# Kernel tuning notes

Measured on AMD Instinct MI355X. Metric: run time of the kernel, lower is better.

The kernel has to match this reference:

```python
import jax, jax.numpy as jnp
import numpy as np

A = 1.0
B = 0.001


def setup_inputs() -> dict:
    key = jax.random.key(0)
    k1, k2 = jax.random.split(key)
    N, C = 4096, 50257
    pred = jax.random.normal(k1, (N, C), dtype=jnp.float32)
    labels = jax.random.randint(k2, (N,), 0, C, dtype=jnp.int64)
    return {"pred": pred, "labels": labels}


def reference(pred, labels):
    N, C = pred.shape
    rows = jnp.arange(N)
    label_logit = pred[rows, labels]  # [N]

    # Cross-entropy (mean reduction, matching nn.CrossEntropyLoss)
    logZ = jax.nn.logsumexp(pred, axis=1)  # [N]
    ce = jnp.mean(logZ - label_logit)

    # Per-row variance-sum over all non-label classes, without building
    # the [N, C] mask / [N, C-1] gather: use sum / sum-of-squares identities.
    # sum_{j != y} (x_j - mu)^2 = sumsq_neg - (C-1) * mu^2
    row_sum = jnp.sum(pred, axis=1) - label_logit            # [N]
    row_sumsq = jnp.sum(pred * pred, axis=1) - label_logit ** 2  # [N]
    m = C - 1
    mu = row_sum / m
    neg_var_sum = jnp.sum(row_sumsq - m * mu * mu)

    return A * ce + B * neg_var_sum
```

## Files before the change

### kernel.cpp

```cpp
#include <hip/hip_runtime.h>
#include <hip/hip_bf16.h>
#include <stdint.h>

#define A_COEF 1.0f
#define B_COEF 0.001f

__device__ __forceinline__ void wave_reduce3(float& a, float& b, float& c) {
    for (int off = 32; off > 0; off >>= 1) {
        a += __shfl_down(a, off);
        b += __shfl_down(b, off);
        c += __shfl_down(c, off);
    }
}

__global__ __launch_bounds__(256) void row_pass_kernel(
    const float* __restrict__ pred, const int* __restrict__ labels,
    float* __restrict__ row_out, int C, float invN) {
    const int row = blockIdx.x;
    const float* __restrict__ p = pred + (size_t)row * (size_t)C;

    const uintptr_t addr = (uintptr_t)p;
    const int head = (int)(((16u - (unsigned)(addr & 15u)) & 15u) >> 2);
    const int nvec = (C - head) >> 2;
    const int tail_start = head + (nvec << 2);

    float sum = 0.0f, ssq = 0.0f, sexp = 0.0f;
    const int t = threadIdx.x;

    for (int i = t; i < head; i += 256) {
        float x = p[i];
        sum += x; ssq = fmaf(x, x, ssq); sexp += __expf(x);
    }
    for (int i = tail_start + t; i < C; i += 256) {
        float x = p[i];
        sum += x; ssq = fmaf(x, x, ssq); sexp += __expf(x);
    }

    const float4* __restrict__ pv = (const float4*)(p + head);
    for (int k = t; k < nvec; k += 256) {
        float4 v = pv[k];
        sum += (v.x + v.y) + (v.z + v.w);
        ssq = fmaf(v.x, v.x, ssq);
        ssq = fmaf(v.y, v.y, ssq);
        ssq = fmaf(v.z, v.z, ssq);
        ssq = fmaf(v.w, v.w, ssq);
        sexp += (__expf(v.x) + __expf(v.y)) + (__expf(v.z) + __expf(v.w));
    }

    __shared__ float s_sum[4], s_ssq[4], s_sexp[4];
    wave_reduce3(sum, ssq, sexp);
    const int wave = t >> 6, lane = t & 63;
    if (lane == 0) { s_sum[wave] = sum; s_ssq[wave] = ssq; s_sexp[wave] = sexp; }
    __syncthreads();

    if (t == 0) {
        float S = 0.0f, Q = 0.0f, E = 0.0f;
        #pragma unroll
        for (int w = 0; w < 4; ++w) { S += s_sum[w]; Q += s_ssq[w]; E += s_sexp[w]; }

        const int label = labels[row];
        const float ll = p[label];

        const float logZ = logf(E);
        const float ce_i = logZ - ll;

        const float m = (float)(C - 1);
        const float rsum = S - ll;
        const float rssq = Q - ll * ll;
        const float mu = rsum / m;
        const float nv = rssq - m * mu * mu;

        row_out[row] = A_COEF * invN * ce_i + B_COEF * nv;
    }
}

__global__ __launch_bounds__(256) void final_reduce_kernel(
    const float* __restrict__ row_out, float* __restrict__ out, int n) {
    double acc = 0.0;
    for (int i = threadIdx.x; i < n; i += 256) acc += (double)row_out[i];
    for (int off = 32; off > 0; off >>= 1) acc += __shfl_down(acc, off);
    __shared__ double sd[4];
    const int wave = threadIdx.x >> 6, lane = threadIdx.x & 63;
    if (lane == 0) sd[wave] = acc;
    __syncthreads();
    if (threadIdx.x == 0) {
        double tot = 0.0;
        #pragma unroll
        for (int w = 0; w < 4; ++w) tot += sd[w];
        out[0] = (float)tot;
    }
}

extern "C" void kernel_launch(void* const* d_in, const int* in_sizes, int n_in,
                              void* d_out, int out_size, void* d_ws, size_t ws_size,
                              hipStream_t stream) {
    const float* pred = (const float*)d_in[0];
    const int* labels = (const int*)d_in[1];
    float* out = (float*)d_out;

    const int N = in_sizes[1];
    const int C = (int)((long long)in_sizes[0] / (long long)N);

    float* row_out = (float*)d_ws;

    row_pass_kernel<<<N, 256, 0, stream>>>(pred, labels, row_out, C, 1.0f / (float)N);
    final_reduce_kernel<<<1, 256, 0, stream>>>(row_out, out, N);
}
```

Before: 150.1 us.

## Fuse final reduction via fixed-point atomics and unroll nontemporal row loads

Removes the second reduction kernel. Each block now adds its row contribution to a 64-bit fixed-point accumulator with an atomic and bumps a counter, and the last block to finish writes the result. The main loop is unrolled by two with separate accumulators and uses nontemporal vector loads, to expose more memory-level parallelism and avoid cache pollution. This adds a memset launch and atomics, and the fixed-point scale limits the precision of each contribution.

```diff
diff --git a/kernel.cpp b/kernel.cpp
--- a/kernel.cpp
+++ b/kernel.cpp
@@ -4,6 +4,9 @@
 
 #define A_COEF 1.0f
 #define B_COEF 0.001f
+#define FIXED_SCALE 16777216.0
+
+typedef __attribute__((ext_vector_type(4))) float f32x4;
 
 __device__ __forceinline__ void wave_reduce3(float& a, float& b, float& c) {
     for (int off = 32; off > 0; off >>= 1) {
@@ -15,7 +18,8 @@
 
 __global__ __launch_bounds__(256) void row_pass_kernel(
     const float* __restrict__ pred, const int* __restrict__ labels,
-    float* __restrict__ row_out, int C, float invN) {
+    unsigned long long* __restrict__ ws, float* __restrict__ out,
+    int C, float invN) {
     const int row = blockIdx.x;
     const float* __restrict__ p = pred + (size_t)row * (size_t)C;
 
@@ -24,28 +28,42 @@
     const int nvec = (C - head) >> 2;
     const int tail_start = head + (nvec << 2);
 
-    float sum = 0.0f, ssq = 0.0f, sexp = 0.0f;
     const int t = threadIdx.x;
+    float sum0 = 0.0f, ssq0 = 0.0f, sexp0 = 0.0f;
+    float sum1 = 0.0f, ssq1 = 0.0f, sexp1 = 0.0f;
 
     for (int i = t; i < head; i += 256) {
         float x = p[i];
-        sum += x; ssq = fmaf(x, x, ssq); sexp += __expf(x);
+        sum0 += x; ssq0 = fmaf(x, x, ssq0); sexp0 += __expf(x);
     }
     for (int i = tail_start + t; i < C; i += 256) {
         float x = p[i];
-        sum += x; ssq = fmaf(x, x, ssq); sexp += __expf(x);
+        sum0 += x; ssq0 = fmaf(x, x, ssq0); sexp0 += __expf(x);
     }
 
-    const float4* __restrict__ pv = (const float4*)(p + head);
-    for (int k = t; k < nvec; k += 256) {
-        float4 v = pv[k];
-        sum += (v.x + v.y) + (v.z + v.w);
-        ssq = fmaf(v.x, v.x, ssq);
-        ssq = fmaf(v.y, v.y, ssq);
-        ssq = fmaf(v.z, v.z, ssq);
-        ssq = fmaf(v.w, v.w, ssq);
-        sexp += (__expf(v.x) + __expf(v.y)) + (__expf(v.z) + __expf(v.w));
+    const f32x4* __restrict__ pv = (const f32x4*)(p + head);
+    int k = t;
+    for (; k + 256 < nvec; k += 512) {
+        f32x4 a = __builtin_nontemporal_load(pv + k);
+        f32x4 b = __builtin_nontemporal_load(pv + k + 256);
+        sum0 += (a[0] + a[1]) + (a[2] + a[3]);
+        sum1 += (b[0] + b[1]) + (b[2] + b[3]);
+        ssq0 = fmaf(a[0], a[0], ssq0); ssq0 = fmaf(a[1], a[1], ssq0);
+        ssq0 = fmaf(a[2], a[2], ssq0); ssq0 = fmaf(a[3], a[3], ssq0);
+        ssq1 = fmaf(b[0], b[0], ssq1); ssq1 = fmaf(b[1], b[1], ssq1);
+        ssq1 = fmaf(b[2], b[2], ssq1); ssq1 = fmaf(b[3], b[3], ssq1);
+        sexp0 += (__expf(a[0]) + __expf(a[1])) + (__expf(a[2]) + __expf(a[3]));
+        sexp1 += (__expf(b[0]) + __expf(b[1])) + (__expf(b[2]) + __expf(b[3]));
     }
+    for (; k < nvec; k += 256) {
+        f32x4 a = __builtin_nontemporal_load(pv + k);
+        sum0 += (a[0] + a[1]) + (a[2] + a[3]);
+        ssq0 = fmaf(a[0], a[0], ssq0); ssq0 = fmaf(a[1], a[1], ssq0);
+        ssq0 = fmaf(a[2], a[2], ssq0); ssq0 = fmaf(a[3], a[3], ssq0);
+        sexp0 += (__expf(a[0]) + __expf(a[1])) + (__expf(a[2]) + __expf(a[3]));
+    }
+
+    float sum = sum0 + sum1, ssq = ssq0 + ssq1, sexp = sexp0 + sexp1;
 
     __shared__ float s_sum[4], s_ssq[4], s_sexp[4];
     wave_reduce3(sum, ssq, sexp);
@@ -70,24 +88,18 @@
         const float mu = rsum / m;
         const float nv = rssq - m * mu * mu;
 
-        row_out[row] = A_COEF * invN * ce_i + B_COEF * nv;
-    }
-}
+        const float contrib = A_COEF * invN * ce_i + B_COEF * nv;
 
-__global__ __launch_bounds__(256) void final_reduce_kernel(
-    const float* __restrict__ row_out, float* __restrict__ out, int n) {
-    double acc = 0.0;
-    for (int i = threadIdx.x; i < n; i += 256) acc += (double)row_out[i];
-    for (int off = 32; off > 0; off >>= 1) acc += __shfl_down(acc, off);
-    __shared__ double sd[4];
-    const int wave = threadIdx.x >> 6, lane = threadIdx.x & 63;
-    if (lane == 0) sd[wave] = acc;
-    __syncthreads();
-    if (threadIdx.x == 0) {
-        double tot = 0.0;
-        #pragma unroll
-        for (int w = 0; w < 4; ++w) tot += sd[w];
-        out[0] = (float)tot;
+        const long long q = (long long)llrint((double)contrib * FIXED_SCALE);
+        atomicAdd(&ws[0], (unsigned long long)q);
+        __threadfence();
+        unsigned int* cnt = (unsigned int*)&ws[1];
+        const unsigned int old = atomicAdd(cnt, 1u);
+        if (old == gridDim.x - 1) {
+            __threadfence();
+            const unsigned long long tot = atomicAdd(&ws[0], 0ULL);
+            out[0] = (float)((double)(long long)tot / FIXED_SCALE);
+        }
     }
 }
 
@@ -101,8 +113,8 @@
     const int N = in_sizes[1];
     const int C = (int)((long long)in_sizes[0] / (long long)N);
 
-    float* row_out = (float*)d_ws;
+    unsigned long long* ws = (unsigned long long*)d_ws;
+    hipMemsetAsync(ws, 0, 16, stream);
 
-    row_pass_kernel<<<N, 256, 0, stream>>>(pred, labels, row_out, C, 1.0f / (float)N);
-    final_reduce_kernel<<<1, 256, 0, stream>>>(row_out, out, N);
+    row_pass_kernel<<<N, 256, 0, stream>>>(pred, labels, ws, out, C, 1.0f / (float)N);
 }
```

Result: slower. 339.2 us (+126.0%).
